# Kernel optimization log

Hardware: AMD Instinct MI355X
Metric: run time of the kernel (lower is better)

The kernel has to match this reference:

```python
import jax, jax.numpy as jnp
import numpy as np

B, C_IN, N = 32, 64, 128
OUT_FEATS = (64, 64, 128)
ATT_DIM = 64
EPS = 1e-5  # torch BatchNorm default


def _bn(x, g, b, m, v):
    # eval-mode BatchNorm over channel axis 1 (running stats m, v)
    shape = (1, -1) + (1,) * (x.ndim - 2)
    inv = g / jnp.sqrt(v + EPS)
    return (x - m.reshape(shape)) * inv.reshape(shape) + b.reshape(shape)


def setup_inputs() -> dict:
    key = jax.random.key(0)
    ks = iter(jax.random.split(key, 48))

    def w(shape, scale=0.05):
        return jax.random.normal(next(ks), shape, jnp.float32) * scale

    inp = {"features": jax.random.normal(next(ks), (B, C_IN, N), jnp.float32)}
    in_dims = (2 * C_IN, OUT_FEATS[0], OUT_FEATS[1])
    for li in range(3):
        o, ci = OUT_FEATS[li], in_dims[li]
        inp[f"w{li}"] = w((o, ci))                  # Conv2d 1x1, no bias (BN)
        inp[f"g{li}"] = 1.0 + w((o,))               # BN gamma
        inp[f"b{li}"] = w((o,))                     # BN beta
        inp[f"m{li}"] = w((o,))                     # BN running mean
        inp[f"v{li}"] = 1.0 + 0.1 * jax.random.uniform(next(ks), (o,), jnp.float32)
    inp["wa0"] = w((ATT_DIM, OUT_FEATS[-1]))        # attention conv (no bias)
    inp["ga"] = 1.0 + w((ATT_DIM,))
    inp["ba"] = w((ATT_DIM,))
    inp["ma"] = w((ATT_DIM,))
    inp["va"] = 1.0 + 0.1 * jax.random.uniform(next(ks), (ATT_DIM,), jnp.float32)
    inp["wa1"] = w((1, ATT_DIM))                    # final attention conv (bias)
    inp["ba1"] = w((1,))
    inp["wsc"] = w((OUT_FEATS[-1], C_IN))           # shortcut Conv1d (no bias)
    inp["gsc"] = 1.0 + w((OUT_FEATS[-1],))
    inp["bsc"] = w((OUT_FEATS[-1],))
    inp["msc"] = w((OUT_FEATS[-1],))
    inp["vsc"] = 1.0 + 0.1 * jax.random.uniform(next(ks), (OUT_FEATS[-1],), jnp.float32)
    return inp


def reference(features, w0, g0, b0, m0, v0, w1, g1, b1, m1, v1,
              w2, g2, b2, m2, v2, wa0, ga, ba, ma, va, wa1, ba1,
              wsc, gsc, bsc, msc, vsc):
    n = features.shape[-1]
    # neighbor index table: row i lists all j != i, shape (N, N-1)
    base = jnp.broadcast_to(jnp.arange(n)[None, :], (n, n))
    idx = jnp.where(base >= jnp.arange(n)[:, None], base + 1, base)[:, :-1]
    x_i = features[:, :, :, None]                   # (B,C,N,1)
    x_j = features[:, :, idx]                       # (B,C,N,N-1) gather
    x = jnp.concatenate([jnp.broadcast_to(x_i, x_j.shape), x_j - x_i], axis=1)  # (B,2C,N,N-1)
    for w_, g_, b_, m_, v_ in ((w0, g0, b0, m0, v0), (w1, g1, b1, m1, v1), (w2, g2, b2, m2, v2)):
        x = jnp.einsum('oc,bcnk->bonk', w_, x)      # 1x1 conv
        x = jax.nn.relu(_bn(x, g_, b_, m_, v_))
    # attention pooling over neighbor axis k
    a = jax.nn.relu(_bn(jnp.einsum('oc,bcnk->bonk', wa0, x), ga, ba, ma, va))
    logits = jnp.einsum('oc,bcnk->bonk', wa1, a) + ba1.reshape(1, 1, 1, 1)
    attw = jax.nn.softmax(logits[:, 0], axis=-1)    # (B,N,N-1)
    fts = jnp.einsum('bcnk,bnk->bcn', x, attw)      # (B,C_out,N)
    # shortcut branch (in_feat != out_feats[-1])
    sc = _bn(jnp.einsum('oc,bcn->bon', wsc, features), gsc, bsc, msc, vsc)
    return jax.nn.relu(sc + fts)
```

## Files before the change

kernel.cpp:

```cpp
#include <hip/hip_runtime.h>

typedef unsigned short u16;
typedef short short8 __attribute__((ext_vector_type(8)));
typedef float floatx4 __attribute__((ext_vector_type(4)));
typedef __bf16 bf16x2 __attribute__((ext_vector_type(2)));

#define MFMA16(a, b, c) __builtin_amdgcn_mfma_f32_16x16x32_bf16((a), (b), (c), 0, 0, 0)

#define W1F_OFF   0u
#define B1F_OFF   8192u
#define W2F_OFF   8448u
#define B2F_OFF   24832u
#define WA0F_OFF  25344u
#define BAF_OFF   41728u
#define WA1F_OFF  41984u
#define BA1F_OFF  42240u
#define P_OFF     42496u
#define Q_OFF     1091072u
#define SC_OFF    2139648u
#define WS_TOTAL  4236800u

__device__ __align__(256) char g_ws[WS_TOTAL];

__device__ __forceinline__ float bits2f(unsigned u) {
  union { unsigned i; float f; } v; v.i = u; return v.f;
}
__device__ __forceinline__ unsigned f2bits(float f) {
  union { float f; unsigned i; } v; v.f = f; return v.i;
}
__device__ __forceinline__ u16 f2bf(float f) {
  return (u16)((f2bits(f) + 0x8000u) >> 16);
}
__device__ __forceinline__ unsigned pack2relu(float a, float b) {
#if __has_builtin(__builtin_amdgcn_cvt_pk_bf16_f32)
  union { bf16x2 h; unsigned u; } cv;
  cv.h = __builtin_amdgcn_cvt_pk_bf16_f32(fmaxf(a, 0.f), fmaxf(b, 0.f));
  return cv.u;
#else
  unsigned lo = (f2bits(fmaxf(a, 0.f)) + 0x8000u) >> 16;
  unsigned hi = (f2bits(fmaxf(b, 0.f)) + 0x8000u) & 0xffff0000u;
  return lo | hi;
#endif
}

__device__ __forceinline__ int sw64(int row, int col) {
  return (row << 6) + ((((col >> 3) ^ (row & 7)) << 3) | (col & 7));
}
__device__ __forceinline__ int sw128(int row, int col) {
  return (row << 7) + ((((col >> 3) ^ (row & 7)) << 3) | (col & 7));
}

__global__ __launch_bounds__(256) void k_pre(
    const float* __restrict__ feat, const float* __restrict__ w0,
    const float* __restrict__ g0, const float* __restrict__ b0, const float* __restrict__ m0, const float* __restrict__ v0,
    const float* __restrict__ w1, const float* __restrict__ g1, const float* __restrict__ b1, const float* __restrict__ m1, const float* __restrict__ v1,
    const float* __restrict__ w2, const float* __restrict__ g2, const float* __restrict__ b2, const float* __restrict__ m2, const float* __restrict__ v2,
    const float* __restrict__ wa0, const float* __restrict__ ga, const float* __restrict__ ba, const float* __restrict__ ma, const float* __restrict__ va,
    const float* __restrict__ wa1, const float* __restrict__ ba1,
    const float* __restrict__ wsc, const float* __restrict__ gsc, const float* __restrict__ bsc, const float* __restrict__ msc, const float* __restrict__ vsc)
{
  __shared__ float smem[9600];
  const int t = threadIdx.x;
  char* ws = g_ws;
  const int blk = blockIdx.x;

  if (blk == 512) {
    float* fs1 = smem; float* fs2 = smem + 64; float* fsa = smem + 192;
    if (t < 64) {
      float s;
      s = g1[t] * rsqrtf(v1[t] + 1e-5f); fs1[t] = s; ((float*)(ws + B1F_OFF))[t] = b1[t] - m1[t] * s;
      s = ga[t] * rsqrtf(va[t] + 1e-5f); fsa[t] = s; ((float*)(ws + BAF_OFF))[t] = ba[t] - ma[t] * s;
      ((float*)(ws + WA1F_OFF))[t] = wa1[t];
    }
    if (t < 128) { float s = g2[t] * rsqrtf(v2[t] + 1e-5f); fs2[t] = s; ((float*)(ws + B2F_OFF))[t] = b2[t] - m2[t] * s; }
    if (t == 0) ((float*)(ws + BA1F_OFF))[0] = ba1[0];
    __syncthreads();
    u16* W1f = (u16*)(ws + W1F_OFF);
    u16* W2f = (u16*)(ws + W2F_OFF);
    u16* Wa0f = (u16*)(ws + WA0F_OFF);
    for (int i = t; i < 4096; i += 256) W1f[i]  = f2bf(fs1[i >> 6] * w1[i]);
    for (int i = t; i < 8192; i += 256) W2f[i]  = f2bf(fs2[i >> 6] * w2[i]);
    for (int i = t; i < 8192; i += 256) Wa0f[i] = f2bf(fsa[i >> 7] * wa0[i]);
    return;
  }

  const int sub = blk & 255;
  const int b = sub >> 3, n0 = (sub & 7) << 4;
  float* Xs  = smem;
  float* Wsm = smem + 1280;

  {
    const int c = t >> 2, j = (t & 3) << 2;
    *(float4*)(Xs + c * 20 + j) = *(const float4*)(feat + b * 8192 + c * 128 + n0 + j);
  }

  if (blk < 256) {
    #pragma unroll
    for (int r = 0; r < 8; r++) {
      const int i = (r * 256 + t) * 4;
      float4 v = *(const float4*)(w0 + i);
      const int o = i >> 7, c = i & 127;
      float* d = Wsm + o * 129 + c;
      d[0] = v.x; d[1] = v.y; d[2] = v.z; d[3] = v.w;
    }
    __syncthreads();
    const int o = t & 63, nb = (t >> 6) << 2;
    const float s  = g0[o] * rsqrtf(v0[o] + 1e-5f);
    const float tt = b0[o] - m0[o] * s;
    const float* wr = Wsm + o * 129;
    float dA0=0.f,dA1=0.f,dA2=0.f,dA3=0.f,dB0=0.f,dB1=0.f,dB2=0.f,dB3=0.f;
    #pragma unroll
    for (int c = 0; c < 64; c++) {
      const float a = wr[c], e = wr[64 + c];
      const float4 x = *(const float4*)(Xs + c * 20 + nb);
      dA0 += a * x.x; dA1 += a * x.y; dA2 += a * x.z; dA3 += a * x.w;
      dB0 += e * x.x; dB1 += e * x.y; dB2 += e * x.z; dB3 += e * x.w;
    }
    float* Pp = (float*)(ws + P_OFF) + (b * 128 + n0 + nb) * 64 + o;
    float* Qp = (float*)(ws + Q_OFF) + (b * 128 + n0 + nb) * 64 + o;
    Pp[0]   = s * dB0; Pp[64]  = s * dB1; Pp[128] = s * dB2; Pp[192] = s * dB3;
    Qp[0]   = s * (dA0 - dB0) + tt; Qp[64]  = s * (dA1 - dB1) + tt;
    Qp[128] = s * (dA2 - dB2) + tt; Qp[192] = s * (dA3 - dB3) + tt;
  } else {
    #pragma unroll
    for (int r = 0; r < 8; r++) {
      const int i = (r * 256 + t) * 4;
      float4 v = *(const float4*)(wsc + i);
      const int o = i >> 6, c = i & 63;
      float* d = Wsm + o * 65 + c;
      d[0] = v.x; d[1] = v.y; d[2] = v.z; d[3] = v.w;
    }
    __syncthreads();
    const int o = t & 127, h = (t >> 7) << 3;
    const float s  = gsc[o] * rsqrtf(vsc[o] + 1e-5f);
    const float tt = bsc[o] - msc[o] * s;
    const float* wr = Wsm + o * 65;
    float d0=0.f,d1=0.f,d2=0.f,d3=0.f,d4=0.f,d5=0.f,d6=0.f,d7=0.f;
    #pragma unroll
    for (int c = 0; c < 64; c++) {
      const float a = wr[c];
      const float4 x0 = *(const float4*)(Xs + c * 20 + h);
      const float4 x1 = *(const float4*)(Xs + c * 20 + h + 4);
      d0 += a * x0.x; d1 += a * x0.y; d2 += a * x0.z; d3 += a * x0.w;
      d4 += a * x1.x; d5 += a * x1.y; d6 += a * x1.z; d7 += a * x1.w;
    }
    float* SCp = (float*)(ws + SC_OFF) + (b * 128 + n0 + h) * 128 + o;
    SCp[0]   = s * d0 + tt; SCp[128] = s * d1 + tt; SCp[256] = s * d2 + tt; SCp[384] = s * d3 + tt;
    SCp[512] = s * d4 + tt; SCp[640] = s * d5 + tt; SCp[768] = s * d6 + tt; SCp[896] = s * d7 + tt;
  }
}

__global__ __launch_bounds__(256, 4) void k_main(float* __restrict__ out)
{
  __shared__ alignas(16) u16 buf[16384];
  __shared__ float parts[4][128];
  __shared__ float attws[128];

  const int blk = blockIdx.x, b = blk >> 7, n = blk & 127, t = threadIdx.x;
  const char* ws = g_ws;
  const float* Pb  = (const float*)(ws + P_OFF);
  const float* Qb  = (const float*)(ws + Q_OFF);
  const float* SCb = (const float*)(ws + SC_OFF);
  const u16*   W1f = (const u16*)(ws + W1F_OFF);
  const float* b1f = (const float*)(ws + B1F_OFF);
  const u16*   W2f = (const u16*)(ws + W2F_OFF);
  const float* b2f = (const float*)(ws + B2F_OFF);
  const u16*   Wa0f= (const u16*)(ws + WA0F_OFF);
  const float* baf = (const float*)(ws + BAF_OFF);
  const float* wa1f= (const float*)(ws + WA1F_OFF);
  const float  ba1v= *(const float*)(ws + BA1F_OFF);

  u16* H0 = buf;
  u16* H1 = buf + 8192;
  u16* H2 = buf;

  const int lane = t & 63, wid = t >> 6, quad = lane >> 4, l16 = lane & 15;
  const int koff = quad * 8;

  const short8 a1w0 = *(const short8*)(W1f + (wid * 16 + l16) * 64 + koff);
  const short8 a1w1 = *(const short8*)(W1f + (wid * 16 + l16) * 64 + 32 + koff);
  const short8 a2w00 = *(const short8*)(W2f + (wid * 32 + l16) * 64 + koff);
  const short8 a2w01 = *(const short8*)(W2f + (wid * 32 + l16) * 64 + 32 + koff);
  const short8 a2w10 = *(const short8*)(W2f + (wid * 32 + 16 + l16) * 64 + koff);
  const short8 a2w11 = *(const short8*)(W2f + (wid * 32 + 16 + l16) * 64 + 32 + koff);

  {
    const int k = t >> 1, half = t & 1;
    const int j = (k < 127) ? ((k < n) ? k : (k + 1)) : n;
    const float4* pr = (const float4*)(Pb + ((b << 7) + j) * 64 + half * 32);
    const float4* qr = (const float4*)(Qb + blk * 64 + half * 32);
    #pragma unroll
    for (int ii = 0; ii < 4; ii++) {
      float4 p0 = pr[2 * ii],     q0 = qr[2 * ii];
      float4 p1 = pr[2 * ii + 1], q1 = qr[2 * ii + 1];
      uint4 sv;
      sv.x = pack2relu(q0.x + p0.x, q0.y + p0.y);
      sv.y = pack2relu(q0.z + p0.z, q0.w + p0.w);
      sv.z = pack2relu(q1.x + p1.x, q1.y + p1.y);
      sv.w = pack2relu(q1.z + p1.z, q1.w + p1.w);
      *(uint4*)(H0 + sw64(k, half * 32 + ii * 8)) = sv;
    }
  }
  __syncthreads();

  {
    const int rr = wid * 16 + quad * 4;
    const float4 bb = *(const float4*)(b1f + rr);
    floatx4 binit; binit[0] = bb.x; binit[1] = bb.y; binit[2] = bb.z; binit[3] = bb.w;
    floatx4 acc[8];
    #pragma unroll
    for (int et = 0; et < 8; et++) acc[et] = binit;
    #pragma unroll
    for (int et = 0; et < 8; et++) {
      const int row = et * 16 + l16;
      short8 bf0 = *(const short8*)(H0 + sw64(row, koff));
      short8 bf1 = *(const short8*)(H0 + sw64(row, koff + 32));
      acc[et] = MFMA16(a1w0, bf0, acc[et]);
      acc[et] = MFMA16(a1w1, bf1, acc[et]);
    }
    #pragma unroll
    for (int et = 0; et < 8; et++) {
      uint2 sv;
      sv.x = pack2relu(acc[et][0], acc[et][1]);
      sv.y = pack2relu(acc[et][2], acc[et][3]);
      *(uint2*)(H1 + sw64(et * 16 + l16, rr)) = sv;
    }
  }
  __syncthreads();

  {
    const int r2 = wid * 32 + quad * 4;
    const float4 bba = *(const float4*)(b2f + r2);
    const float4 bbb = *(const float4*)(b2f + r2 + 16);
    floatx4 ia; ia[0] = bba.x; ia[1] = bba.y; ia[2] = bba.z; ia[3] = bba.w;
    floatx4 ib; ib[0] = bbb.x; ib[1] = bbb.y; ib[2] = bbb.z; ib[3] = bbb.w;
    floatx4 acc[2][8];
    #pragma unroll
    for (int et = 0; et < 8; et++) { acc[0][et] = ia; acc[1][et] = ib; }
    #pragma unroll
    for (int et = 0; et < 8; et++) {
      const int row = et * 16 + l16;
      short8 bf0 = *(const short8*)(H1 + sw64(row, koff));
      short8 bf1 = *(const short8*)(H1 + sw64(row, koff + 32));
      acc[0][et] = MFMA16(a2w00, bf0, acc[0][et]);
      acc[0][et] = MFMA16(a2w01, bf1, acc[0][et]);
      acc[1][et] = MFMA16(a2w10, bf0, acc[1][et]);
      acc[1][et] = MFMA16(a2w11, bf1, acc[1][et]);
    }
    __syncthreads();
    #pragma unroll
    for (int m = 0; m < 2; m++) {
      const int rr = r2 + m * 16;
      #pragma unroll
      for (int et = 0; et < 8; et++) {
        uint2 sv;
        sv.x = pack2relu(acc[m][et][0], acc[m][et][1]);
        sv.y = pack2relu(acc[m][et][2], acc[m][et][3]);
        *(uint2*)(H2 + sw128(et * 16 + l16, rr)) = sv;
      }
    }
  }

  short8 a3[4];
  #pragma unroll
  for (int ks = 0; ks < 4; ks++)
    a3[ks] = *(const short8*)(Wa0f + (wid * 16 + l16) * 128 + ks * 32 + koff);

  __syncthreads();

  float scv = 0.f;
  if (t < 128) scv = SCb[blk * 128 + t];
  float* outp = out + ((b << 7) + (t & 127)) * 128 + n;

  {
    const int rr = wid * 16 + quad * 4;
    const float4 bb = *(const float4*)(baf + rr);
    const float4 wv = *(const float4*)(wa1f + rr);
    floatx4 binit; binit[0] = bb.x; binit[1] = bb.y; binit[2] = bb.z; binit[3] = bb.w;
    floatx4 acc[8];
    #pragma unroll
    for (int et = 0; et < 8; et++) acc[et] = binit;
    #pragma unroll
    for (int et = 0; et < 8; et++) {
      const int row = et * 16 + l16;
      #pragma unroll
      for (int ks = 0; ks < 4; ks++) {
        short8 bf = *(const short8*)(H2 + sw128(row, koff + ks * 32));
        acc[et] = MFMA16(a3[ks], bf, acc[et]);
      }
    }
    #pragma unroll
    for (int et = 0; et < 8; et++) {
      float p = wv.x * fmaxf(acc[et][0], 0.f) + wv.y * fmaxf(acc[et][1], 0.f)
              + wv.z * fmaxf(acc[et][2], 0.f) + wv.w * fmaxf(acc[et][3], 0.f);
      p += __shfl_xor(p, 16); p += __shfl_xor(p, 32);
      if (quad == 0) parts[wid][et * 16 + l16] = p;
    }
  }

  const int chg = t & 15, eg = t >> 4;
  uint4 hv[8];
  #pragma unroll
  for (int i = 0; i < 8; i++)
    hv[i] = *(const uint4*)(H2 + sw128(eg * 8 + i, chg * 8));

  __syncthreads();

  if (wid == 0) {
    float a0 = parts[0][lane] + parts[1][lane] + parts[2][lane] + parts[3][lane] + ba1v;
    float a1 = (lane == 63) ? -1e30f
             : (parts[0][lane + 64] + parts[1][lane + 64] + parts[2][lane + 64] + parts[3][lane + 64] + ba1v);
    float mx = fmaxf(a0, a1);
    #pragma unroll
    for (int off = 32; off >= 1; off >>= 1) mx = fmaxf(mx, __shfl_xor(mx, off));
    float e0 = expf(a0 - mx), e1 = expf(a1 - mx);
    float sm = e0 + e1;
    #pragma unroll
    for (int off = 32; off >= 1; off >>= 1) sm += __shfl_xor(sm, off);
    float inv = 1.f / sm;
    attws[lane] = e0 * inv;
    attws[lane + 64] = e1 * inv;
  }
  __syncthreads();

  {
    float fa[8];
    #pragma unroll
    for (int k = 0; k < 8; k++) fa[k] = 0.f;
    #pragma unroll
    for (int i = 0; i < 8; i++) {
      const float w = attws[eg * 8 + i];
      uint4 v = hv[i];
      unsigned u;
      u = v.x; fa[0] += w * bits2f(u << 16); fa[1] += w * bits2f(u & 0xffff0000u);
      u = v.y; fa[2] += w * bits2f(u << 16); fa[3] += w * bits2f(u & 0xffff0000u);
      u = v.z; fa[4] += w * bits2f(u << 16); fa[5] += w * bits2f(u & 0xffff0000u);
      u = v.w; fa[6] += w * bits2f(u << 16); fa[7] += w * bits2f(u & 0xffff0000u);
    }
    #pragma unroll
    for (int k = 0; k < 8; k++) { fa[k] += __shfl_xor(fa[k], 16); fa[k] += __shfl_xor(fa[k], 32); }
    if (lane < 16) {
      #pragma unroll
      for (int k = 0; k < 8; k++) parts[wid][chg * 8 + k] = fa[k];
    }
  }
  __syncthreads();

  if (t < 128) {
    float fts = parts[0][t] + parts[1][t] + parts[2][t] + parts[3][t];
    *outp = fmaxf(scv + fts, 0.f);
  }
}

extern "C" void kernel_launch(void* const* d_in, const int* in_sizes, int n_in,
                              void* d_out, int out_size, void* d_ws, size_t ws_size,
                              hipStream_t stream)
{
  (void)d_ws; (void)ws_size; (void)in_sizes; (void)n_in; (void)out_size;
  const float* feat = (const float*)d_in[0];
  const float *w0 = (const float*)d_in[1],  *g0 = (const float*)d_in[2],  *b0 = (const float*)d_in[3],  *m0 = (const float*)d_in[4],  *v0 = (const float*)d_in[5];
  const float *w1 = (const float*)d_in[6],  *g1 = (const float*)d_in[7],  *b1 = (const float*)d_in[8],  *m1 = (const float*)d_in[9],  *v1 = (const float*)d_in[10];
  const float *w2 = (const float*)d_in[11], *g2 = (const float*)d_in[12], *b2 = (const float*)d_in[13], *m2 = (const float*)d_in[14], *v2 = (const float*)d_in[15];
  const float *wa0= (const float*)d_in[16], *ga = (const float*)d_in[17], *ba = (const float*)d_in[18], *ma = (const float*)d_in[19], *va = (const float*)d_in[20];
  const float *wa1= (const float*)d_in[21], *ba1= (const float*)d_in[22];
  const float *wsc= (const float*)d_in[23], *gsc= (const float*)d_in[24], *bsc= (const float*)d_in[25], *msc= (const float*)d_in[26], *vsc= (const float*)d_in[27];

  k_pre<<<dim3(513), dim3(256), 0, stream>>>(
      feat, w0, g0, b0, m0, v0, w1, g1, b1, m1, v1, w2, g2, b2, m2, v2,
      wa0, ga, ba, ma, va, wa1, ba1, wsc, gsc, bsc, msc, vsc);
  k_main<<<dim3(4096), dim3(256), 0, stream>>>((float*)d_out);
}
```

Measured before the change: 168.5 us.

## Split neighbor axis into two halves with online softmax to shrink LDS

Processes the 128 neighbor rows in two passes of 64 and merges the attention softmax across halves with a running max and sum, as in online softmax. LDS per block drops from 32KB to 24KB, and launch bounds rise from 4 to 6 blocks per SM. Every wave now computes the softmax redundantly instead of only wave 0. The cost is more __syncthreads per block, roughly twice as many barrier phases, and extra exp rescaling, in exchange for higher occupancy and lower register pressure.

```diff
diff --git a/kernel.cpp b/kernel.cpp
--- a/kernel.cpp
+++ b/kernel.cpp
@@ -150,11 +150,10 @@
   }
 }
 
-__global__ __launch_bounds__(256, 4) void k_main(float* __restrict__ out)
+__global__ __launch_bounds__(256, 6) void k_main(float* __restrict__ out)
 {
-  __shared__ alignas(16) u16 buf[16384];
+  __shared__ alignas(16) u16 buf[12288];
   __shared__ float parts[4][128];
-  __shared__ float attws[128];
 
   const int blk = blockIdx.x, b = blk >> 7, n = blk & 127, t = threadIdx.x;
   const char* ws = g_ws;
@@ -170,12 +169,13 @@
   const float* wa1f= (const float*)(ws + WA1F_OFF);
   const float  ba1v= *(const float*)(ws + BA1F_OFF);
 
-  u16* H0 = buf;
-  u16* H1 = buf + 8192;
-  u16* H2 = buf;
+  u16* RA = buf;
+  u16* RB = buf + 4096;
+  u16* RC = buf + 8192;
 
   const int lane = t & 63, wid = t >> 6, quad = lane >> 4, l16 = lane & 15;
   const int koff = quad * 8;
+  const int chg = t & 15, eg = t >> 4;
 
   const short8 a1w0 = *(const short8*)(W1f + (wid * 16 + l16) * 64 + koff);
   const short8 a1w1 = *(const short8*)(W1f + (wid * 16 + l16) * 64 + 32 + koff);
@@ -184,159 +184,173 @@
   const short8 a2w10 = *(const short8*)(W2f + (wid * 32 + 16 + l16) * 64 + koff);
   const short8 a2w11 = *(const short8*)(W2f + (wid * 32 + 16 + l16) * 64 + 32 + koff);
 
-  {
-    const int k = t >> 1, half = t & 1;
-    const int j = (k < 127) ? ((k < n) ? k : (k + 1)) : n;
-    const float4* pr = (const float4*)(Pb + ((b << 7) + j) * 64 + half * 32);
-    const float4* qr = (const float4*)(Qb + blk * 64 + half * 32);
-    #pragma unroll
-    for (int ii = 0; ii < 4; ii++) {
-      float4 p0 = pr[2 * ii],     q0 = qr[2 * ii];
-      float4 p1 = pr[2 * ii + 1], q1 = qr[2 * ii + 1];
-      uint4 sv;
-      sv.x = pack2relu(q0.x + p0.x, q0.y + p0.y);
-      sv.y = pack2relu(q0.z + p0.z, q0.w + p0.w);
-      sv.z = pack2relu(q1.x + p1.x, q1.y + p1.y);
-      sv.w = pack2relu(q1.z + p1.z, q1.w + p1.w);
-      *(uint4*)(H0 + sw64(k, half * 32 + ii * 8)) = sv;
-    }
-  }
-  __syncthreads();
-
-  {
-    const int rr = wid * 16 + quad * 4;
-    const float4 bb = *(const float4*)(b1f + rr);
-    floatx4 binit; binit[0] = bb.x; binit[1] = bb.y; binit[2] = bb.z; binit[3] = bb.w;
-    floatx4 acc[8];
-    #pragma unroll
-    for (int et = 0; et < 8; et++) acc[et] = binit;
-    #pragma unroll
-    for (int et = 0; et < 8; et++) {
-      const int row = et * 16 + l16;
-      short8 bf0 = *(const short8*)(H0 + sw64(row, koff));
-      short8 bf1 = *(const short8*)(H0 + sw64(row, koff + 32));
-      acc[et] = MFMA16(a1w0, bf0, acc[et]);
-      acc[et] = MFMA16(a1w1, bf1, acc[et]);
-    }
-    #pragma unroll
-    for (int et = 0; et < 8; et++) {
-      uint2 sv;
-      sv.x = pack2relu(acc[et][0], acc[et][1]);
-      sv.y = pack2relu(acc[et][2], acc[et][3]);
-      *(uint2*)(H1 + sw64(et * 16 + l16, rr)) = sv;
-    }
-  }
-  __syncthreads();
-
-  {
-    const int r2 = wid * 32 + quad * 4;
-    const float4 bba = *(const float4*)(b2f + r2);
-    const float4 bbb = *(const float4*)(b2f + r2 + 16);
-    floatx4 ia; ia[0] = bba.x; ia[1] = bba.y; ia[2] = bba.z; ia[3] = bba.w;
-    floatx4 ib; ib[0] = bbb.x; ib[1] = bbb.y; ib[2] = bbb.z; ib[3] = bbb.w;
-    floatx4 acc[2][8];
-    #pragma unroll
-    for (int et = 0; et < 8; et++) { acc[0][et] = ia; acc[1][et] = ib; }
-    #pragma unroll
-    for (int et = 0; et < 8; et++) {
-      const int row = et * 16 + l16;
-      short8 bf0 = *(const short8*)(H1 + sw64(row, koff));
-      short8 bf1 = *(const short8*)(H1 + sw64(row, koff + 32));
-      acc[0][et] = MFMA16(a2w00, bf0, acc[0][et]);
-      acc[0][et] = MFMA16(a2w01, bf1, acc[0][et]);
-      acc[1][et] = MFMA16(a2w10, bf0, acc[1][et]);
-      acc[1][et] = MFMA16(a2w11, bf1, acc[1][et]);
-    }
-    __syncthreads();
-    #pragma unroll
-    for (int m = 0; m < 2; m++) {
-      const int rr = r2 + m * 16;
-      #pragma unroll
-      for (int et = 0; et < 8; et++) {
-        uint2 sv;
-        sv.x = pack2relu(acc[m][et][0], acc[m][et][1]);
-        sv.y = pack2relu(acc[m][et][2], acc[m][et][3]);
-        *(uint2*)(H2 + sw128(et * 16 + l16, rr)) = sv;
-      }
-    }
-  }
-
-  short8 a3[4];
-  #pragma unroll
-  for (int ks = 0; ks < 4; ks++)
-    a3[ks] = *(const short8*)(Wa0f + (wid * 16 + l16) * 128 + ks * 32 + koff);
-
-  __syncthreads();
-
   float scv = 0.f;
   if (t < 128) scv = SCb[blk * 128 + t];
   float* outp = out + ((b << 7) + (t & 127)) * 128 + n;
 
+  float mx_run = 0.f, s_run = 0.f;
+  float fa[8];
+  #pragma unroll
+  for (int k = 0; k < 8; k++) fa[k] = 0.f;
+
+  #pragma unroll
+  for (int h = 0; h < 2; h++) {
+    {
+      const int k = t >> 2, q4 = t & 3;
+      const int egl = h * 64 + k;
+      const int j = (egl < 127) ? ((egl < n) ? egl : (egl + 1)) : n;
+      const float4* pr = (const float4*)(Pb + ((b << 7) + j) * 64 + q4 * 16);
+      const float4* qr = (const float4*)(Qb + blk * 64 + q4 * 16);
+      float4 p0 = pr[0], p1 = pr[1], p2 = pr[2], p3 = pr[3];
+      float4 q0 = qr[0], q1 = qr[1], q2 = qr[2], q3 = qr[3];
+      uint4 s0, s1;
+      s0.x = pack2relu(q0.x + p0.x, q0.y + p0.y);
+      s0.y = pack2relu(q0.z + p0.z, q0.w + p0.w);
+      s0.z = pack2relu(q1.x + p1.x, q1.y + p1.y);
+      s0.w = pack2relu(q1.z + p1.z, q1.w + p1.w);
+      s1.x = pack2relu(q2.x + p2.x, q2.y + p2.y);
+      s1.y = pack2relu(q2.z + p2.z, q2.w + p2.w);
+      s1.z = pack2relu(q3.x + p3.x, q3.y + p3.y);
+      s1.w = pack2relu(q3.z + p3.z, q3.w + p3.w);
+      *(uint4*)(RA + sw64(k, q4 * 16))     = s0;
+      *(uint4*)(RA + sw64(k, q4 * 16 + 8)) = s1;
+    }
+    __syncthreads();
+
+    {
+      const int rr = wid * 16 + quad * 4;
+      const float4 bb = *(const float4*)(b1f + rr);
+      floatx4 binit; binit[0] = bb.x; binit[1] = bb.y; binit[2] = bb.z; binit[3] = bb.w;
+      floatx4 acc[4];
+      #pragma unroll
+      for (int et = 0; et < 4; et++) acc[et] = binit;
+      #pragma unroll
+      for (int et = 0; et < 4; et++) {
+        const int row = et * 16 + l16;
+        short8 bf0 = *(const short8*)(RA + sw64(row, koff));
+        short8 bf1 = *(const short8*)(RA + sw64(row, koff + 32));
+        acc[et] = MFMA16(a1w0, bf0, acc[et]);
+        acc[et] = MFMA16(a1w1, bf1, acc[et]);
+      }
+      #pragma unroll
+      for (int et = 0; et < 4; et++) {
+        uint2 sv;
+        sv.x = pack2relu(acc[et][0], acc[et][1]);
+        sv.y = pack2relu(acc[et][2], acc[et][3]);
+        *(uint2*)(RC + sw64(et * 16 + l16, rr)) = sv;
+      }
+    }
+    __syncthreads();
+
+    {
+      const int r2 = wid * 32 + quad * 4;
+      const float4 bba = *(const float4*)(b2f + r2);
+      const float4 bbb = *(const float4*)(b2f + r2 + 16);
+      floatx4 ia; ia[0] = bba.x; ia[1] = bba.y; ia[2] = bba.z; ia[3] = bba.w;
+      floatx4 ib; ib[0] = bbb.x; ib[1] = bbb.y; ib[2] = bbb.z; ib[3] = bbb.w;
+      floatx4 acc[2][4];
+      #pragma unroll
+      for (int et = 0; et < 4; et++) { acc[0][et] = ia; acc[1][et] = ib; }
+      #pragma unroll
+      for (int et = 0; et < 4; et++) {
+        const int row = et * 16 + l16;
+        short8 bf0 = *(const short8*)(RC + sw64(row, koff));
+        short8 bf1 = *(const short8*)(RC + sw64(row, koff + 32));
+        acc[0][et] = MFMA16(a2w00, bf0, acc[0][et]);
+        acc[0][et] = MFMA16(a2w01, bf1, acc[0][et]);
+        acc[1][et] = MFMA16(a2w10, bf0, acc[1][et]);
+        acc[1][et] = MFMA16(a2w11, bf1, acc[1][et]);
+      }
+      #pragma unroll
+      for (int m = 0; m < 2; m++) {
+        const int cc = r2 + m * 16;
+        #pragma unroll
+        for (int et = 0; et < 4; et++) {
+          uint2 sv;
+          sv.x = pack2relu(acc[m][et][0], acc[m][et][1]);
+          sv.y = pack2relu(acc[m][et][2], acc[m][et][3]);
+          if (et < 2) *(uint2*)(RB + sw128(et * 16 + l16, cc)) = sv;
+          else        *(uint2*)(RA + sw128((et - 2) * 16 + l16, cc)) = sv;
+        }
+      }
+    }
+
+    short8 a3[4];
+    #pragma unroll
+    for (int ks = 0; ks < 4; ks++)
+      a3[ks] = *(const short8*)(Wa0f + (wid * 16 + l16) * 128 + ks * 32 + koff);
+
+    __syncthreads();
+
+    {
+      const int rr = wid * 16 + quad * 4;
+      const float4 bb = *(const float4*)(baf + rr);
+      const float4 wv = *(const float4*)(wa1f + rr);
+      floatx4 binit; binit[0] = bb.x; binit[1] = bb.y; binit[2] = bb.z; binit[3] = bb.w;
+      #pragma unroll
+      for (int et = 0; et < 4; et++) {
+        const int row = et * 16 + l16;
+        const u16* hb = (et < 2) ? RB : RA;
+        const int rrow = row & 31;
+        floatx4 ac = binit;
+        #pragma unroll
+        for (int ks = 0; ks < 4; ks++) {
+          short8 bf = *(const short8*)(hb + sw128(rrow, koff + ks * 32));
+          ac = MFMA16(a3[ks], bf, ac);
+        }
+        float p = wv.x * fmaxf(ac[0], 0.f) + wv.y * fmaxf(ac[1], 0.f)
+                + wv.z * fmaxf(ac[2], 0.f) + wv.w * fmaxf(ac[3], 0.f);
+        p += __shfl_xor(p, 16); p += __shfl_xor(p, 32);
+        if (quad == 0) parts[wid][et * 16 + l16] = p;
+      }
+    }
+
+    uint4 hv[4];
+    #pragma unroll
+    for (int i = 0; i < 4; i++) {
+      const int e = eg * 4 + i;
+      const u16* hb = (eg < 8) ? RB : RA;
+      hv[i] = *(const uint4*)(hb + sw128(e & 31, chg * 8));
+    }
+
+    __syncthreads();
+
+    {
+      float a = parts[0][lane] + parts[1][lane] + parts[2][lane] + parts[3][lane] + ba1v;
+      if (h == 1 && lane == 63) a = -1e30f;
+      float mxh = a;
+      #pragma unroll
+      for (int off = 32; off >= 1; off >>= 1) mxh = fmaxf(mxh, __shfl_xor(mxh, off));
+      const float mxn = (h == 0) ? mxh : fmaxf(mx_run, mxh);
+      const float f   = (h == 0) ? 1.f : expf(mx_run - mxn);
+      const float w   = expf(a - mxn);
+      float sh = w;
+      #pragma unroll
+      for (int off = 32; off >= 1; off >>= 1) sh += __shfl_xor(sh, off);
+      s_run = (h == 0) ? sh : s_run * f + sh;
+      mx_run = mxn;
+
+      if (h == 1) {
+        #pragma unroll
+        for (int k = 0; k < 8; k++) fa[k] *= f;
+      }
+      #pragma unroll
+      for (int i = 0; i < 4; i++) {
+        const float wv = __shfl(w, eg * 4 + i);
+        uint4 v = hv[i];
+        unsigned u;
+        u = v.x; fa[0] += wv * bits2f(u << 16); fa[1] += wv * bits2f(u & 0xffff0000u);
+        u = v.y; fa[2] += wv * bits2f(u << 16); fa[3] += wv * bits2f(u & 0xffff0000u);
+        u = v.z; fa[4] += wv * bits2f(u << 16); fa[5] += wv * bits2f(u & 0xffff0000u);
+        u = v.w; fa[6] += wv * bits2f(u << 16); fa[7] += wv * bits2f(u & 0xffff0000u);
+      }
+    }
+  }
+
+  const float inv = 1.f / s_run;
+
+  __syncthreads();
   {
-    const int rr = wid * 16 + quad * 4;
-    const float4 bb = *(const float4*)(baf + rr);
-    const float4 wv = *(const float4*)(wa1f + rr);
-    floatx4 binit; binit[0] = bb.x; binit[1] = bb.y; binit[2] = bb.z; binit[3] = bb.w;
-    floatx4 acc[8];
-    #pragma unroll
-    for (int et = 0; et < 8; et++) acc[et] = binit;
-    #pragma unroll
-    for (int et = 0; et < 8; et++) {
-      const int row = et * 16 + l16;
-      #pragma unroll
-      for (int ks = 0; ks < 4; ks++) {
-        short8 bf = *(const short8*)(H2 + sw128(row, koff + ks * 32));
-        acc[et] = MFMA16(a3[ks], bf, acc[et]);
-      }
-    }
-    #pragma unroll
-    for (int et = 0; et < 8; et++) {
-      float p = wv.x * fmaxf(acc[et][0], 0.f) + wv.y * fmaxf(acc[et][1], 0.f)
-              + wv.z * fmaxf(acc[et][2], 0.f) + wv.w * fmaxf(acc[et][3], 0.f);
-      p += __shfl_xor(p, 16); p += __shfl_xor(p, 32);
-      if (quad == 0) parts[wid][et * 16 + l16] = p;
-    }
-  }
-
-  const int chg = t & 15, eg = t >> 4;
-  uint4 hv[8];
-  #pragma unroll
-  for (int i = 0; i < 8; i++)
-    hv[i] = *(const uint4*)(H2 + sw128(eg * 8 + i, chg * 8));
-
-  __syncthreads();
-
-  if (wid == 0) {
-    float a0 = parts[0][lane] + parts[1][lane] + parts[2][lane] + parts[3][lane] + ba1v;
-    float a1 = (lane == 63) ? -1e30f
-             : (parts[0][lane + 64] + parts[1][lane + 64] + parts[2][lane + 64] + parts[3][lane + 64] + ba1v);
-    float mx = fmaxf(a0, a1);
-    #pragma unroll
-    for (int off = 32; off >= 1; off >>= 1) mx = fmaxf(mx, __shfl_xor(mx, off));
-    float e0 = expf(a0 - mx), e1 = expf(a1 - mx);
-    float sm = e0 + e1;
-    #pragma unroll
-    for (int off = 32; off >= 1; off >>= 1) sm += __shfl_xor(sm, off);
-    float inv = 1.f / sm;
-    attws[lane] = e0 * inv;
-    attws[lane + 64] = e1 * inv;
-  }
-  __syncthreads();
-
-  {
-    float fa[8];
-    #pragma unroll
-    for (int k = 0; k < 8; k++) fa[k] = 0.f;
-    #pragma unroll
-    for (int i = 0; i < 8; i++) {
-      const float w = attws[eg * 8 + i];
-      uint4 v = hv[i];
-      unsigned u;
-      u = v.x; fa[0] += w * bits2f(u << 16); fa[1] += w * bits2f(u & 0xffff0000u);
-      u = v.y; fa[2] += w * bits2f(u << 16); fa[3] += w * bits2f(u & 0xffff0000u);
-      u = v.z; fa[4] += w * bits2f(u << 16); fa[5] += w * bits2f(u & 0xffff0000u);
-      u = v.w; fa[6] += w * bits2f(u << 16); fa[7] += w * bits2f(u & 0xffff0000u);
-    }
     #pragma unroll
     for (int k = 0; k < 8; k++) { fa[k] += __shfl_xor(fa[k], 16); fa[k] += __shfl_xor(fa[k], 32); }
     if (lane < 16) {
@@ -348,7 +362,7 @@
 
   if (t < 128) {
     float fts = parts[0][t] + parts[1][t] + parts[2][t] + parts[3][t];
-    *outp = fmaxf(scv + fts, 0.f);
+    *outp = fmaxf(scv + fts * inv, 0.f);
   }
 }
 
```

Result: slower. 221.9 us (+31.7%).
